# Performance work log

Measured on AMD Instinct MI355X. Metric: run time of the kernel, lower is better.

## Reference

```python
import jax, jax.numpy as jnp
import numpy as np

H = 1024
W = 1024
N = 4194304


def setup_inputs() -> dict:
    key = jax.random.key(0)
    k1, k2 = jax.random.split(key)
    inputs = jax.random.uniform(k1, (N, 2), dtype=jnp.float32)  # query points (x, v)
    grid = jax.random.normal(k2, (H, W), dtype=jnp.float32)     # 2-D lookup table f(x, v)
    bounds = jnp.array([[0.0, 1.0], [0.0, 1.0]], dtype=jnp.float32)  # [[x_lo,x_hi],[v_lo,v_hi]]
    return {"inputs": inputs, "grid": grid, "bounds": bounds}


def _axis_coords(q, size):
    # TF _interpolate_bilinear: floor clamped to [0, size-2], alpha clamped to [0, 1]
    fl = jnp.clip(jnp.floor(q), 0.0, size - 2.0)
    alpha = jnp.clip(q - fl, 0.0, 1.0)
    return fl.astype(jnp.int32), alpha


def reference(inputs, grid, bounds):
    h = jnp.float32(grid.shape[0])
    w = jnp.float32(grid.shape[1])
    # normalized fractional indices (ij indexing: dim0 = x-row, dim1 = v-col)
    qy = (h - 1.0) * (inputs[:, 0] - bounds[0, 0]) / (bounds[0, 1] - bounds[0, 0])
    qx = (w - 1.0) * (inputs[:, 1] - bounds[1, 0]) / (bounds[1, 1] - bounds[1, 0])
    y0, ay = _axis_coords(qy, grid.shape[0])
    x0, ax = _axis_coords(qx, grid.shape[1])
    # 4-point gather + bilinear blend
    tl = grid[y0, x0]
    tr = grid[y0, x0 + 1]
    bl = grid[y0 + 1, x0]
    br = grid[y0 + 1, x0 + 1]
    top = tl + (tr - tl) * ax
    bot = bl + (br - bl) * ax
    out = top + (bot - top) * ay
    return out[None, :, None]  # [1, N, 1] to match _interpolate_bilinear output
```

## Files before the change

### kernel.cpp

```cpp
#include <hip/hip_runtime.h>


#ifndef GRID_H
#define GRID_H 1024
#define GRID_W 1024
#endif

typedef float floatx4 __attribute__((ext_vector_type(4)));
typedef float floatx2 __attribute__((ext_vector_type(2)));

__global__ __launch_bounds__(256) void tableInterp_kernel(
    const float* __restrict__ in,
    const float* __restrict__ grid,
    const float* __restrict__ bounds,
    float* __restrict__ out,
    int n_pts)
{
    const int H = GRID_H, W = GRID_W;
    const float x_lo = bounds[0];
    const float x_hi = bounds[1];
    const float v_lo = bounds[2];
    const float v_hi = bounds[3];
    const float sy = (float)(H - 1) / (x_hi - x_lo);
    const float sx = (float)(W - 1) / (v_hi - v_lo);

    const int t = blockIdx.x * blockDim.x + threadIdx.x;
    const int base = t * 4;
    if (base >= n_pts) return;

    float xs[4], vs[4], res[4];

    if (base + 3 < n_pts) {
        const floatx4* in4 = (const floatx4*)in;
        floatx4 p01 = __builtin_nontemporal_load(&in4[2 * t + 0]);
        floatx4 p23 = __builtin_nontemporal_load(&in4[2 * t + 1]);
        xs[0] = p01.x; vs[0] = p01.y;
        xs[1] = p01.z; vs[1] = p01.w;
        xs[2] = p23.x; vs[2] = p23.y;
        xs[3] = p23.z; vs[3] = p23.w;
    } else {
#pragma unroll
        for (int k = 0; k < 4; ++k) {
            int p = base + k < n_pts ? base + k : n_pts - 1;
            xs[k] = in[2 * p + 0];
            vs[k] = in[2 * p + 1];
        }
    }

    float ays[4], axs[4];
    const floatx2* gtop[4];
    const floatx2* gbot[4];

#pragma unroll
    for (int k = 0; k < 4; ++k) {
        float qy = (xs[k] - x_lo) * sy;
        float qx = (vs[k] - v_lo) * sx;
        float fy = fminf(fmaxf(floorf(qy), 0.0f), (float)(H - 2));
        float fx = fminf(fmaxf(floorf(qx), 0.0f), (float)(W - 2));
        ays[k] = fminf(fmaxf(qy - fy, 0.0f), 1.0f);
        axs[k] = fminf(fmaxf(qx - fx, 0.0f), 1.0f);
        int y0 = (int)fy;
        int x0 = (int)fx;
        const float* g = grid + (y0 * W + x0);
        gtop[k] = (const floatx2*)g;
        gbot[k] = (const floatx2*)(g + W);
    }

    floatx2 top2[4], bot2[4];
#pragma unroll
    for (int k = 0; k < 4; ++k) {
        top2[k] = *gtop[k];
        bot2[k] = *gbot[k];
    }

#pragma unroll
    for (int k = 0; k < 4; ++k) {
        float top = top2[k].x + (top2[k].y - top2[k].x) * axs[k];
        float bot = bot2[k].x + (bot2[k].y - bot2[k].x) * axs[k];
        res[k] = top + (bot - top) * ays[k];
    }

    if (base + 3 < n_pts) {
        floatx4 o;
        o.x = res[0]; o.y = res[1]; o.z = res[2]; o.w = res[3];
        __builtin_nontemporal_store(o, &((floatx4*)out)[t]);
    } else {
#pragma unroll
        for (int k = 0; k < 4; ++k)
            if (base + k < n_pts) out[base + k] = res[k];
    }
}

extern "C" void kernel_launch(void* const* d_in, const int* in_sizes, int n_in,
                              void* d_out, int out_size, void* d_ws, size_t ws_size,
                              hipStream_t stream) {
    const float* in     = (const float*)d_in[0];
    const float* grid   = (const float*)d_in[1];
    const float* bounds = (const float*)d_in[2];
    float* out = (float*)d_out;

    const int n_pts = in_sizes[0] / 2;
    const int n_threads = (n_pts + 3) / 4;
    const int block = 256;
    const int blocks = (n_threads + block - 1) / block;
    tableInterp_kernel<<<blocks, block, 0, stream>>>(in, grid, bounds, out, n_pts);
}
```

Baseline: 126.1 us.

## Precompute per-cell quad table so each query does one 16-byte gather

Adds a pre-pass kernel that builds a workspace table holding the four corner values of every grid cell as a float4. The interpolation kernel then does a single 16-byte gather per point instead of two 8-byte gathers from separate rows, and each thread now handles 8 points. The goal is fewer scattered memory transactions per query. In exchange there is an extra launch that writes a 16 MB table (four times the grid) rebuilt on every call, and the gather footprint grows. A fallback raw kernel runs when the workspace is too small.

```diff
diff --git a/kernel.cpp b/kernel.cpp
--- a/kernel.cpp
+++ b/kernel.cpp
@@ -1,17 +1,32 @@
 #include <hip/hip_runtime.h>
 
 
-#ifndef GRID_H
 #define GRID_H 1024
 #define GRID_W 1024
-#endif
 
 typedef float floatx4 __attribute__((ext_vector_type(4)));
 typedef float floatx2 __attribute__((ext_vector_type(2)));
 
-__global__ __launch_bounds__(256) void tableInterp_kernel(
+__global__ __launch_bounds__(256) void buildQuad_kernel(
+    const float* __restrict__ grid,
+    floatx4* __restrict__ quad,
+    int n_entries)
+{
+    int idx = blockIdx.x * blockDim.x + threadIdx.x;
+    if (idx >= n_entries) return;
+    int y = idx >> 10;
+    int x = idx & (GRID_W - 1);
+    int x1 = x + 1 < GRID_W ? x + 1 : GRID_W - 1;
+    const float* r0 = grid + (y << 10);
+    const float* r1 = r0 + GRID_W;
+    floatx4 q;
+    q.x = r0[x]; q.y = r0[x1]; q.z = r1[x]; q.w = r1[x1];
+    quad[idx] = q;
+}
+
+__global__ __launch_bounds__(256) void interpQuad_kernel(
     const float* __restrict__ in,
-    const float* __restrict__ grid,
+    const floatx4* __restrict__ quad,
     const float* __restrict__ bounds,
     float* __restrict__ out,
     int n_pts)
@@ -25,32 +40,89 @@
     const float sx = (float)(W - 1) / (v_hi - v_lo);
 
     const int t = blockIdx.x * blockDim.x + threadIdx.x;
-    const int base = t * 4;
+    const int base = t * 8;
     if (base >= n_pts) return;
 
-    float xs[4], vs[4], res[4];
+    float xs[8], vs[8], res[8];
 
-    if (base + 3 < n_pts) {
+    if (base + 7 < n_pts) {
         const floatx4* in4 = (const floatx4*)in;
-        floatx4 p01 = __builtin_nontemporal_load(&in4[2 * t + 0]);
-        floatx4 p23 = __builtin_nontemporal_load(&in4[2 * t + 1]);
-        xs[0] = p01.x; vs[0] = p01.y;
-        xs[1] = p01.z; vs[1] = p01.w;
-        xs[2] = p23.x; vs[2] = p23.y;
-        xs[3] = p23.z; vs[3] = p23.w;
+#pragma unroll
+        for (int q = 0; q < 4; ++q) {
+            floatx4 p = __builtin_nontemporal_load(&in4[4 * t + q]);
+            xs[2 * q + 0] = p.x; vs[2 * q + 0] = p.y;
+            xs[2 * q + 1] = p.z; vs[2 * q + 1] = p.w;
+        }
     } else {
 #pragma unroll
-        for (int k = 0; k < 4; ++k) {
+        for (int k = 0; k < 8; ++k) {
             int p = base + k < n_pts ? base + k : n_pts - 1;
             xs[k] = in[2 * p + 0];
             vs[k] = in[2 * p + 1];
         }
     }
 
+    float ays[8], axs[8];
+    int qidx[8];
+#pragma unroll
+    for (int k = 0; k < 8; ++k) {
+        float qy = (xs[k] - x_lo) * sy;
+        float qx = (vs[k] - v_lo) * sx;
+        float fy = fminf(fmaxf(floorf(qy), 0.0f), (float)(H - 2));
+        float fx = fminf(fmaxf(floorf(qx), 0.0f), (float)(W - 2));
+        ays[k] = fminf(fmaxf(qy - fy, 0.0f), 1.0f);
+        axs[k] = fminf(fmaxf(qx - fx, 0.0f), 1.0f);
+        qidx[k] = ((int)fy << 10) + (int)fx;
+    }
+
+    floatx4 c[8];
+#pragma unroll
+    for (int k = 0; k < 8; ++k) c[k] = quad[qidx[k]];
+
+#pragma unroll
+    for (int k = 0; k < 8; ++k) {
+        float top = c[k].x + (c[k].y - c[k].x) * axs[k];
+        float bot = c[k].z + (c[k].w - c[k].z) * axs[k];
+        res[k] = top + (bot - top) * ays[k];
+    }
+
+    if (base + 7 < n_pts) {
+        floatx4* out4 = (floatx4*)out;
+#pragma unroll
+        for (int q = 0; q < 2; ++q) {
+            floatx4 o;
+            o.x = res[4 * q + 0]; o.y = res[4 * q + 1];
+            o.z = res[4 * q + 2]; o.w = res[4 * q + 3];
+            __builtin_nontemporal_store(o, &out4[2 * t + q]);
+        }
+    } else {
+#pragma unroll
+        for (int k = 0; k < 8; ++k)
+            if (base + k < n_pts) out[base + k] = res[k];
+    }
+}
+
+__global__ __launch_bounds__(256) void interpRaw_kernel(
+    const float* __restrict__ in, const float* __restrict__ grid,
+    const float* __restrict__ bounds, float* __restrict__ out, int n_pts)
+{
+    const int H = GRID_H, W = GRID_W;
+    const float x_lo = bounds[0], x_hi = bounds[1];
+    const float v_lo = bounds[2], v_hi = bounds[3];
+    const float sy = (float)(H - 1) / (x_hi - x_lo);
+    const float sx = (float)(W - 1) / (v_hi - v_lo);
+    const int t = blockIdx.x * blockDim.x + threadIdx.x;
+    const int base = t * 4;
+    if (base >= n_pts) return;
+    float xs[4], vs[4], res[4];
+#pragma unroll
+    for (int k = 0; k < 4; ++k) {
+        int p = base + k < n_pts ? base + k : n_pts - 1;
+        xs[k] = in[2 * p + 0];
+        vs[k] = in[2 * p + 1];
+    }
     float ays[4], axs[4];
-    const floatx2* gtop[4];
-    const floatx2* gbot[4];
-
+    const floatx2 *gt[4], *gb[4];
 #pragma unroll
     for (int k = 0; k < 4; ++k) {
         float qy = (xs[k] - x_lo) * sy;
@@ -59,36 +131,22 @@
         float fx = fminf(fmaxf(floorf(qx), 0.0f), (float)(W - 2));
         ays[k] = fminf(fmaxf(qy - fy, 0.0f), 1.0f);
         axs[k] = fminf(fmaxf(qx - fx, 0.0f), 1.0f);
-        int y0 = (int)fy;
-        int x0 = (int)fx;
-        const float* g = grid + (y0 * W + x0);
-        gtop[k] = (const floatx2*)g;
-        gbot[k] = (const floatx2*)(g + W);
+        const float* g = grid + ((int)fy << 10) + (int)fx;
+        gt[k] = (const floatx2*)g;
+        gb[k] = (const floatx2*)(g + W);
     }
-
-    floatx2 top2[4], bot2[4];
+    floatx2 t2[4], b2[4];
+#pragma unroll
+    for (int k = 0; k < 4; ++k) { t2[k] = *gt[k]; b2[k] = *gb[k]; }
 #pragma unroll
     for (int k = 0; k < 4; ++k) {
-        top2[k] = *gtop[k];
-        bot2[k] = *gbot[k];
-    }
-
-#pragma unroll
-    for (int k = 0; k < 4; ++k) {
-        float top = top2[k].x + (top2[k].y - top2[k].x) * axs[k];
-        float bot = bot2[k].x + (bot2[k].y - bot2[k].x) * axs[k];
+        float top = t2[k].x + (t2[k].y - t2[k].x) * axs[k];
+        float bot = b2[k].x + (b2[k].y - b2[k].x) * axs[k];
         res[k] = top + (bot - top) * ays[k];
     }
-
-    if (base + 3 < n_pts) {
-        floatx4 o;
-        o.x = res[0]; o.y = res[1]; o.z = res[2]; o.w = res[3];
-        __builtin_nontemporal_store(o, &((floatx4*)out)[t]);
-    } else {
 #pragma unroll
-        for (int k = 0; k < 4; ++k)
-            if (base + k < n_pts) out[base + k] = res[k];
-    }
+    for (int k = 0; k < 4; ++k)
+        if (base + k < n_pts) out[base + k] = res[k];
 }
 
 extern "C" void kernel_launch(void* const* d_in, const int* in_sizes, int n_in,
@@ -100,8 +158,18 @@
     float* out = (float*)d_out;
 
     const int n_pts = in_sizes[0] / 2;
-    const int n_threads = (n_pts + 3) / 4;
-    const int block = 256;
-    const int blocks = (n_threads + block - 1) / block;
-    tableInterp_kernel<<<blocks, block, 0, stream>>>(in, grid, bounds, out, n_pts);
+    const int n_quad = (GRID_H - 1) * GRID_W;
+    const size_t quad_bytes = (size_t)n_quad * 16;
+
+    if (ws_size >= quad_bytes) {
+        floatx4* quad = (floatx4*)d_ws;
+        buildQuad_kernel<<<(n_quad + 255) / 256, 256, 0, stream>>>(grid, quad, n_quad);
+        const int n_threads = (n_pts + 7) / 8;
+        interpQuad_kernel<<<(n_threads + 255) / 256, 256, 0, stream>>>(
+            in, quad, bounds, out, n_pts);
+    } else {
+        const int n_threads = (n_pts + 3) / 4;
+        interpRaw_kernel<<<(n_threads + 255) / 256, 256, 0, stream>>>(
+            in, grid, bounds, out, n_pts);
+    }
 }
```

Result: slower. 151.6 us (+20.3%).
